# Kernel tuning notes

Hardware: AMD Instinct MI355X
Metric: run time of the kernel (lower is better)

Reference implementation:

```python
import jax, jax.numpy as jnp
import numpy as np

GROUPS = 4

def shuffle(t):
    # torch Shuffle: transpose(-1,-2).contiguous().view(original_shape)
    return jnp.swapaxes(t, -1, -2).reshape(t.shape)

def setup_inputs() -> dict:
    key = jax.random.key(0)
    B, H = 131072, 512
    gh = 2 * H // GROUPS  # 256
    k = jax.random.split(key, 5)
    s = lambda fan_in: 1.0 / np.sqrt(fan_in)
    x = jax.random.normal(k[0], (B, H), dtype=jnp.float32)
    # weights stored as (in, out); Linear has bias=False throughout
    W1 = jax.random.uniform(k[1], (H, H), jnp.float32, -s(H), s(H))
    W2 = jax.random.uniform(k[2], (gh, gh), jnp.float32, -s(gh), s(gh))
    W3 = jax.random.uniform(k[3], (gh, gh), jnp.float32, -s(gh), s(gh))
    W4 = jax.random.uniform(k[4], (2 * H, H), jnp.float32, -s(2 * H), s(2 * H))
    return {"x": x, "W1": W1, "W2": W2, "W3": W3, "W4": W4}

def reference(x, W1, W2, W3, W4):
    B, H = x.shape
    gh = 2 * H // GROUPS
    sorted_x = jnp.sort(x, axis=1, stable=True)
    h = jnp.stack((x, sorted_x), axis=1)          # (B, 2, H)
    h = h @ W1                                    # (B, 2, H)
    h = h.reshape(B, GROUPS, gh)                  # Flatten + Unflatten
    h = shuffle(h)
    h = h @ W2                                    # (B, GROUPS, gh)
    h = shuffle(h)
    h = jax.nn.relu(h @ W3)                       # (B, GROUPS, gh)
    h = h.reshape(B, GROUPS * gh)                 # (B, 2H)
    scores = jax.nn.sigmoid(h @ W4)               # (B, H)
    return x * scores
```

## Files before the change

### kernel.cpp

```cpp
#include <hip/hip_runtime.h>
#include <hip/hip_bf16.h>
#include <cstdint>
#include <cstddef>

typedef short bf16x8 __attribute__((ext_vector_type(8)));
typedef float f32x4 __attribute__((ext_vector_type(4)));

#define BM 256
#define BN 128
#define BK 64

__device__ __forceinline__ void gl_lds16(const __hip_bfloat16* gp, __hip_bfloat16* lp) {
  __builtin_amdgcn_global_load_lds((const __attribute__((address_space(1))) void*)gp,
                                   (__attribute__((address_space(3))) void*)lp, 16, 0, 0);
}

__global__ void __launch_bounds__(256) wtrans_kernel(const float* __restrict__ src,
                                                     __hip_bfloat16* __restrict__ dst,
                                                     int R, int C) {
  int idx = blockIdx.x * 256 + threadIdx.x;
  if (idx >= R * C) return;
  int r = idx / C, c = idx % C;
  dst[(size_t)c * R + r] = __float2bfloat16(src[idx]);
}

__global__ void __launch_bounds__(256) sort_kernel(const float* __restrict__ x,
                                                   __hip_bfloat16* __restrict__ h0) {
  int row = blockIdx.x * 4 + (threadIdx.x >> 6);
  int lane = threadIdx.x & 63;
  const float* xr = x + (size_t)row * 512;

  float v[8];
  *(float4*)&v[0] = *(const float4*)&xr[lane * 8];
  *(float4*)&v[4] = *(const float4*)&xr[lane * 8 + 4];

  __hip_bfloat16* h = h0 + (size_t)row * 1024;
  {
    alignas(16) __hip_bfloat16 ob[8];
#pragma unroll
    for (int i = 0; i < 8; ++i) ob[i] = __float2bfloat16(v[i]);
    *(bf16x8*)&h[lane * 8] = *(const bf16x8*)ob;
  }

#pragma unroll
  for (int k = 2; k <= 512; k <<= 1) {
#pragma unroll
    for (int j = k >> 1; j > 0; j >>= 1) {
      if (j >= 8) {
        int L = j >> 3;
        bool lower = (lane & L) == 0;
        bool up = (((lane * 8) & k) == 0);
        bool sel = (lower == up);
#pragma unroll
        for (int r = 0; r < 8; ++r) {
          float pv = __shfl_xor(v[r], L, 64);
          float mn = fminf(v[r], pv), mx = fmaxf(v[r], pv);
          v[r] = sel ? mn : mx;
        }
      } else {
#pragma unroll
        for (int r = 0; r < 8; ++r) {
          if ((r & j) == 0) {
            int r2 = r | j;
            bool up = ((((lane * 8) + r) & k) == 0);
            float a = v[r], b = v[r2];
            float mn = fminf(a, b), mx = fmaxf(a, b);
            v[r] = up ? mn : mx;
            v[r2] = up ? mx : mn;
          }
        }
      }
    }
  }

  {
    alignas(16) __hip_bfloat16 ob[8];
#pragma unroll
    for (int i = 0; i < 8; ++i) ob[i] = __float2bfloat16(v[i]);
    *(bf16x8*)&h[512 + lane * 8] = *(const bf16x8*)ob;
  }
}

template <int EPI, int N, int K>
__global__ void __launch_bounds__(512) gemm_k(const __hip_bfloat16* __restrict__ A,
                                              const __hip_bfloat16* __restrict__ BT,
                                              __hip_bfloat16* __restrict__ Cb,
                                              float* __restrict__ Co,
                                              const float* __restrict__ X) {
  __shared__ __hip_bfloat16 lA[3][BM * BK];
  __shared__ __hip_bfloat16 lB[3][BN * BK];

  int nwg = gridDim.x;
  int bid = blockIdx.x;
  int cpx = nwg >> 3;
  int wg = (bid & 7) * cpx + (bid >> 3);

  constexpr int NTN = N / BN;
  int m0 = (wg / NTN) * BM;
  int n0 = (wg % NTN) * BN;

  int tid = threadIdx.x;
  int lane = tid & 63;
  int w = tid >> 6;
  int wr = w >> 1;
  int wc = w & 1;
  int r16 = lane & 15;
  int g4 = lane >> 4;

  int ar = lane >> 3;
  int acs = 8 * ((lane & 7) ^ (ar & 7));
  const __hip_bfloat16* Asrc = A + (size_t)(m0 + w * 32 + ar) * K + acs;
  const __hip_bfloat16* Bsrc = BT + (size_t)(n0 + w * 16 + ar) * K + acs;

  int xorr = (r16 & 7) * 8;
  int arow[4], brow[4];
#pragma unroll
  for (int i = 0; i < 4; ++i) arow[i] = (wr * 64 + 16 * i + r16) * BK;
#pragma unroll
  for (int j = 0; j < 4; ++j) brow[j] = (wc * 64 + 16 * j + r16) * BK;
  int kx0 = (g4 * 8) ^ xorr;
  int kx1 = (32 + g4 * 8) ^ xorr;

  f32x4 acc[4][4] = {};

#define STAGE(tt, bb)                                                     \
  do {                                                                    \
    int k0_ = (tt) * BK;                                                  \
    gl_lds16(Asrc + k0_, &lA[bb][(w * 4 + 0) * 512]);                     \
    gl_lds16(Asrc + (size_t)8 * K + k0_, &lA[bb][(w * 4 + 1) * 512]);     \
    gl_lds16(Asrc + (size_t)16 * K + k0_, &lA[bb][(w * 4 + 2) * 512]);    \
    gl_lds16(Asrc + (size_t)24 * K + k0_, &lA[bb][(w * 4 + 3) * 512]);    \
    gl_lds16(Bsrc + k0_, &lB[bb][(w * 2 + 0) * 512]);                     \
    gl_lds16(Bsrc + (size_t)8 * K + k0_, &lB[bb][(w * 2 + 1) * 512]);     \
  } while (0)

  constexpr int NT = K / BK;
  STAGE(0, 0);
  STAGE(1, 1);
  asm volatile("s_waitcnt vmcnt(6)" ::: "memory");
  __builtin_amdgcn_s_barrier();

#pragma unroll
  for (int t = 0; t < NT; ++t) {
    const int cur = t % 3;
    const int nxt = (t + 2) % 3;

    bf16x8 a0[4], b0[4];
#pragma unroll
    for (int i = 0; i < 4; ++i) a0[i] = *(const bf16x8*)&lA[cur][arow[i] + kx0];
#pragma unroll
    for (int j = 0; j < 4; ++j) b0[j] = *(const bf16x8*)&lB[cur][brow[j] + kx0];

    if (t + 2 < NT) STAGE(t + 2, nxt);

    __builtin_amdgcn_s_setprio(1);
#pragma unroll
    for (int i = 0; i < 4; ++i)
#pragma unroll
      for (int j = 0; j < 4; ++j)
        acc[i][j] = __builtin_amdgcn_mfma_f32_16x16x32_bf16(a0[i], b0[j], acc[i][j], 0, 0, 0);
    __builtin_amdgcn_s_setprio(0);

    bf16x8 a1[4], b1[4];
#pragma unroll
    for (int i = 0; i < 4; ++i) a1[i] = *(const bf16x8*)&lA[cur][arow[i] + kx1];
#pragma unroll
    for (int j = 0; j < 4; ++j) b1[j] = *(const bf16x8*)&lB[cur][brow[j] + kx1];

    __builtin_amdgcn_s_setprio(1);
#pragma unroll
    for (int i = 0; i < 4; ++i)
#pragma unroll
      for (int j = 0; j < 4; ++j)
        acc[i][j] = __builtin_amdgcn_mfma_f32_16x16x32_bf16(a1[i], b1[j], acc[i][j], 0, 0, 0);
    __builtin_amdgcn_s_setprio(0);

    if (t + 1 < NT) {
      if (t + 2 < NT) asm volatile("s_waitcnt vmcnt(6)" ::: "memory");
      else            asm volatile("s_waitcnt vmcnt(0)" ::: "memory");
      __builtin_amdgcn_s_barrier();
    }
  }
#undef STAGE

#pragma unroll
  for (int i = 0; i < 4; ++i) {
    int grow_base = m0 + wr * 64 + 16 * i + g4 * 4;
#pragma unroll
    for (int j = 0; j < 4; ++j) {
      int gcol = n0 + wc * 64 + 16 * j + r16;
#pragma unroll
      for (int r = 0; r < 4; ++r) {
        int grow = grow_base + r;
        float v = acc[i][j][r];
        if constexpr (EPI == 1) {
          int b = grow >> 1, p = grow & 1;
          Cb[(size_t)b * 1024 + 4 * (gcol & 255) + (p << 1) + (gcol >> 8)] = __float2bfloat16(v);
        } else if constexpr (EPI == 2) {
          int b = grow >> 2, g = grow & 3;
          Cb[(size_t)b * 1024 + 4 * gcol + g] = __float2bfloat16(v);
        } else if constexpr (EPI == 3) {
          Cb[(size_t)grow * N + gcol] = __float2bfloat16(fmaxf(v, 0.f));
        } else {
          float xv = X[(size_t)grow * N + gcol];
          Co[(size_t)grow * N + gcol] = xv / (1.f + __expf(-v));
        }
      }
    }
  }
}

extern "C" void kernel_launch(void* const* d_in, const int* in_sizes, int n_in,
                              void* d_out, int out_size, void* d_ws, size_t ws_size,
                              hipStream_t stream) {
  const float* x  = (const float*)d_in[0];
  const float* W1 = (const float*)d_in[1];
  const float* W2 = (const float*)d_in[2];
  const float* W3 = (const float*)d_in[3];
  const float* W4 = (const float*)d_in[4];

  const int B = 131072;

  char* ws = (char*)d_ws;
  __hip_bfloat16* W1T = (__hip_bfloat16*)(ws);
  __hip_bfloat16* W2T = (__hip_bfloat16*)(ws + 524288);
  __hip_bfloat16* W3T = (__hip_bfloat16*)(ws + 655360);
  __hip_bfloat16* W4T = (__hip_bfloat16*)(ws + 786432);
  __hip_bfloat16* bufA = (__hip_bfloat16*)(ws + 2097152);
  __hip_bfloat16* bufB = bufA + (size_t)134217728;

  wtrans_kernel<<<(512 * 512) / 256, 256, 0, stream>>>(W1, W1T, 512, 512);
  wtrans_kernel<<<(256 * 256) / 256, 256, 0, stream>>>(W2, W2T, 256, 256);
  wtrans_kernel<<<(256 * 256) / 256, 256, 0, stream>>>(W3, W3T, 256, 256);
  wtrans_kernel<<<(1024 * 512) / 256, 256, 0, stream>>>(W4, W4T, 1024, 512);

  sort_kernel<<<B / 4, 256, 0, stream>>>(x, bufA);

  gemm_k<1, 512, 512><<<(2 * B / BM) * (512 / BN), 512, 0, stream>>>(bufA, W1T, bufB, nullptr, nullptr);
  gemm_k<2, 256, 256><<<(4 * B / BM) * (256 / BN), 512, 0, stream>>>(bufB, W2T, bufA, nullptr, nullptr);
  gemm_k<3, 256, 256><<<(4 * B / BM) * (256 / BN), 512, 0, stream>>>(bufA, W3T, bufB, nullptr, nullptr);
  gemm_k<4, 512, 1024><<<(B / BM) * (512 / BN), 512, 0, stream>>>(bufB, W4T, nullptr, (float*)d_out, x);
}
```

Measured before the change: 1.108 ms.

## Stage GEMM A tiles through registers with deeper global prefetch

The A operand no longer uses direct global-to-LDS loads. Each thread reads contiguous 16-byte chunks into a triple-buffered register array up to four k-tiles ahead, then writes them to LDS with the XOR swizzle on the LDS side. B keeps the direct global_load_lds path. The goal is to make A's global reads coalesced and deepen the prefetch to hide memory latency. The cost is extra VGPRs, extra LDS write instructions and added lgkmcnt waits before each barrier.

New measurement: 1.139 ms. 1.03x slower.

```diff
diff --git a/kernel.cpp b/kernel.cpp
--- a/kernel.cpp
+++ b/kernel.cpp
@@ -107,10 +107,13 @@
   int r16 = lane & 15;
   int g4 = lane >> 4;
 
-  int ar = lane >> 3;
-  int acs = 8 * ((lane & 7) ^ (ar & 7));
-  const __hip_bfloat16* Asrc = A + (size_t)(m0 + w * 32 + ar) * K + acs;
-  const __hip_bfloat16* Bsrc = BT + (size_t)(n0 + w * 16 + ar) * K + acs;
+  int lr = lane >> 3;
+  int lc = (lane & 7) * 8;
+  int wcol = 8 * ((lane & 7) ^ lr);
+  const __hip_bfloat16* Ag = A + (size_t)(m0 + w * 32 + lr) * K + lc;
+
+  int acs = 8 * ((lane & 7) ^ lr);
+  const __hip_bfloat16* Bsrc = BT + (size_t)(n0 + w * 16 + lr) * K + acs;
 
   int xorr = (r16 & 7) * 8;
   int arow[4], brow[4];
@@ -122,36 +125,56 @@
   int kx1 = (32 + g4 * 8) ^ xorr;
 
   f32x4 acc[4][4] = {};
-
-#define STAGE(tt, bb)                                                     \
-  do {                                                                    \
-    int k0_ = (tt) * BK;                                                  \
-    gl_lds16(Asrc + k0_, &lA[bb][(w * 4 + 0) * 512]);                     \
-    gl_lds16(Asrc + (size_t)8 * K + k0_, &lA[bb][(w * 4 + 1) * 512]);     \
-    gl_lds16(Asrc + (size_t)16 * K + k0_, &lA[bb][(w * 4 + 2) * 512]);    \
-    gl_lds16(Asrc + (size_t)24 * K + k0_, &lA[bb][(w * 4 + 3) * 512]);    \
-    gl_lds16(Bsrc + k0_, &lB[bb][(w * 2 + 0) * 512]);                     \
-    gl_lds16(Bsrc + (size_t)8 * K + k0_, &lB[bb][(w * 2 + 1) * 512]);     \
+  bf16x8 ra[3][4];
+
+#define LOADA(tt)                                                       \
+  do {                                                                  \
+    const int k0_ = (tt) * BK, b_ = (tt) % 3;                           \
+    ra[b_][0] = *(const bf16x8*)(Ag + k0_);                             \
+    ra[b_][1] = *(const bf16x8*)(Ag + (size_t)8 * K + k0_);             \
+    ra[b_][2] = *(const bf16x8*)(Ag + (size_t)16 * K + k0_);            \
+    ra[b_][3] = *(const bf16x8*)(Ag + (size_t)24 * K + k0_);            \
   } while (0)
 
+#define WRITEA(tt)                                                      \
+  do {                                                                  \
+    const int b_ = (tt) % 3;                                            \
+    *(bf16x8*)&lA[b_][(w * 32 + 0 + lr) * BK + wcol] = ra[b_][0];       \
+    *(bf16x8*)&lA[b_][(w * 32 + 8 + lr) * BK + wcol] = ra[b_][1];       \
+    *(bf16x8*)&lA[b_][(w * 32 + 16 + lr) * BK + wcol] = ra[b_][2];      \
+    *(bf16x8*)&lA[b_][(w * 32 + 24 + lr) * BK + wcol] = ra[b_][3];      \
+  } while (0)
+
+#define STAGEB(tt)                                                      \
+  do {                                                                  \
+    const int k0_ = (tt) * BK, b_ = (tt) % 3;                           \
+    gl_lds16(Bsrc + k0_, &lB[b_][(w * 2 + 0) * 512]);                   \
+    gl_lds16(Bsrc + (size_t)8 * K + k0_, &lB[b_][(w * 2 + 1) * 512]);   \
+  } while (0)
+
   constexpr int NT = K / BK;
-  STAGE(0, 0);
-  STAGE(1, 1);
+  LOADA(0); LOADA(1); LOADA(2);
+  STAGEB(0); STAGEB(1);
+  asm volatile("s_waitcnt vmcnt(8)" ::: "memory");
+  WRITEA(0); WRITEA(1);
+  LOADA(3);
   asm volatile("s_waitcnt vmcnt(6)" ::: "memory");
+  asm volatile("s_waitcnt lgkmcnt(0)" ::: "memory");
   __builtin_amdgcn_s_barrier();
 
 #pragma unroll
   for (int t = 0; t < NT; ++t) {
     const int cur = t % 3;
-    const int nxt = (t + 2) % 3;
+
+    if (t + 2 < NT) STAGEB(t + 2);
+    if (t + 4 < NT) LOADA(t + 4);
+    if (t + 2 < NT) WRITEA(t + 2);
 
     bf16x8 a0[4], b0[4];
 #pragma unroll
     for (int i = 0; i < 4; ++i) a0[i] = *(const bf16x8*)&lA[cur][arow[i] + kx0];
 #pragma unroll
     for (int j = 0; j < 4; ++j) b0[j] = *(const bf16x8*)&lB[cur][brow[j] + kx0];
-
-    if (t + 2 < NT) STAGE(t + 2, nxt);
 
     __builtin_amdgcn_s_setprio(1);
 #pragma unroll
@@ -176,12 +199,16 @@
     __builtin_amdgcn_s_setprio(0);
 
     if (t + 1 < NT) {
-      if (t + 2 < NT) asm volatile("s_waitcnt vmcnt(6)" ::: "memory");
-      else            asm volatile("s_waitcnt vmcnt(0)" ::: "memory");
+      if (t + 4 < NT)      asm volatile("s_waitcnt vmcnt(6)" ::: "memory");
+      else if (t + 2 < NT) asm volatile("s_waitcnt vmcnt(2)" ::: "memory");
+      else                 asm volatile("s_waitcnt vmcnt(0)" ::: "memory");
+      asm volatile("s_waitcnt lgkmcnt(0)" ::: "memory");
       __builtin_amdgcn_s_barrier();
     }
   }
-#undef STAGE
+#undef LOADA
+#undef WRITEA
+#undef STAGEB
 
 #pragma unroll
   for (int i = 0; i < 4; ++i) {
```
